# Performance work log

Measured on AMD Instinct MI355X. Metric: run time of the kernel, lower is better.

Reference implementation:

```python
import jax, jax.numpy as jnp
import numpy as np

EMBED_DIM = 768
NUM_HEADS = 12
HEAD_DIM = EMBED_DIM // NUM_HEADS  # 64
SEGMENT_LENGTHS = (2048, 4096, 8192)
DILATION_RATES = (1, 2, 4)
LN_EPS = 1e-5


def setup_inputs() -> dict:
    key = jax.random.key(0)
    ks = jax.random.split(key, 8)
    B, N, E = 2, 8192, EMBED_DIM
    std = 1.0 / np.sqrt(E)
    return {
        "query": jax.random.normal(ks[0], (B, N, E), jnp.float32),
        "key": jax.random.normal(ks[1], (B, N, E), jnp.float32),
        "value": jax.random.normal(ks[2], (B, N, E), jnp.float32),
        "Wqkv": jax.random.normal(ks[3], (3 * E, E), jnp.float32) * std,
        "bqkv": jnp.zeros((3 * E,), jnp.float32),
        "Wo": jax.random.normal(ks[4], (E, E), jnp.float32) * std,
        "bo": jnp.zeros((E,), jnp.float32),
        "ln_w": jnp.ones((E,), jnp.float32),
        "ln_b": jnp.zeros((E,), jnp.float32),
        "is_causal": 0,
    }


def _dilated_attention(q, k, v, is_causal):
    # q, k, v: (b, n, h, d). Heads are partitioned into len(SEGMENT_LENGTHS) groups.
    b, n, h, d = q.shape
    ng = len(SEGMENT_LENGTHS)
    g = h // ng  # heads per group
    scale = 1.0 / np.sqrt(d)
    outs = []
    for i, (s, r) in enumerate(zip(SEGMENT_LENGTHS, DILATION_RATES)):
        off = i % r
        hs = slice(i * g, (i + 1) * g)
        m = n // s          # number of segments
        t = (s - off + r - 1) // r  # dilated tokens per segment
        # (b, m, s, g, d) -> dilated subsample -> (b, m, t, g, d)
        qi = q[:, :, hs].reshape(b, m, s, g, d)[:, :, off::r] * scale
        ki = k[:, :, hs].reshape(b, m, s, g, d)[:, :, off::r]
        vi = v[:, :, hs].reshape(b, m, s, g, d)[:, :, off::r]
        # attention within each segment over the dilated tokens
        scores = jnp.einsum("bmqhd,bmkhd->bmhqk", qi, ki)  # (b,m,g,t,t)
        if is_causal:
            mask = jnp.tril(jnp.ones((t, t), bool))
            scores = jnp.where(mask, scores, jnp.finfo(scores.dtype).min)
        attn = jax.nn.softmax(scores, axis=-1)
        xi = jnp.einsum("bmhqk,bmkhd->bmqhd", attn, vi)  # (b,m,t,g,d)
        # scatter back into full segment positions (zeros elsewhere)
        full = jnp.zeros((b, m, s, g, d), xi.dtype).at[:, :, off::r].set(xi)
        outs.append(full.reshape(b, n, g, d))
    return jnp.concatenate(outs, axis=2)  # (b, n, h, d)


def reference(query, key, value, Wqkv, bqkv, Wo, bo, ln_w, ln_b, is_causal):
    b, n, e = query.shape
    h, d = NUM_HEADS, HEAD_DIM
    q = (query @ Wqkv[:e].T + bqkv[:e]).reshape(b, n, h, d)
    k = (key @ Wqkv[e:2 * e].T + bqkv[e:2 * e]).reshape(b, n, h, d)
    v = (value @ Wqkv[2 * e:].T + bqkv[2 * e:]).reshape(b, n, h, d)
    x = _dilated_attention(q, k, v, is_causal).reshape(b, n, e)
    # LayerNorm
    mu = jnp.mean(x, axis=-1, keepdims=True)
    var = jnp.mean(jnp.square(x - mu), axis=-1, keepdims=True)
    x = (x - mu) * jax.lax.rsqrt(var + LN_EPS) * ln_w + ln_b
    return x @ Wo.T + bo
```

## Files before the change

### kernel.cpp

```cpp
#include <hip/hip_runtime.h>
#include <stdint.h>
#include <stddef.h>

typedef __bf16 bf16;
typedef __attribute__((ext_vector_type(4))) float f32x4;
typedef __attribute__((ext_vector_type(16))) float f32x16;
typedef __attribute__((ext_vector_type(8))) bf16 bf16x8;
typedef __attribute__((ext_vector_type(4))) bf16 bf16x4;

#define INST_STRIDE (2048 * 64)

static __device__ __forceinline__ f32x4 mfma16(bf16x8 a, bf16x8 b, f32x4 c) {
  return __builtin_amdgcn_mfma_f32_16x16x32_bf16(a, b, c, 0, 0, 0);
}
static __device__ __forceinline__ f32x16 mfma32(bf16x8 a, bf16x8 b, f32x16 c) {
  return __builtin_amdgcn_mfma_f32_32x32x16_bf16(a, b, c, 0, 0, 0);
}
static __device__ __forceinline__ void gload16(const void* g, void* l) {
  __builtin_amdgcn_global_load_lds(
      (const __attribute__((address_space(1))) void*)g,
      (__attribute__((address_space(3))) void*)l, 16, 0, 0);
}

__global__ void convert_w(const float* __restrict__ Wqkv, const float* __restrict__ Wo,
                          bf16* __restrict__ wq, bf16* __restrict__ wo) {
  int idx = blockIdx.x * 256 + threadIdx.x;
  const int NQ = 3 * 768 * 768 / 4;
  const float4* src;
  bf16* dst;
  int i;
  if (idx < NQ) { src = (const float4*)Wqkv; dst = wq; i = idx; }
  else          { src = (const float4*)Wo;   dst = wo; i = idx - NQ; }
  float4 v = src[i];
  bf16x4 o = { (bf16)v.x, (bf16)v.y, (bf16)v.z, (bf16)v.w };
  *(bf16x4*)(dst + (size_t)i * 4) = o;
}

__launch_bounds__(512, 2)
__global__ void qkv_gemm(const float* __restrict__ Xq, const float* __restrict__ Xk,
                         const float* __restrict__ Xv, const bf16* __restrict__ Wb,
                         const float* __restrict__ bqkv, bf16* __restrict__ qg,
                         bf16* __restrict__ kg, bf16* __restrict__ vtg) {
  __shared__ __align__(16) bf16 lA[128 * 64];
  __shared__ __align__(16) bf16 lB[256 * 64];
  const int z = blockIdx.z;
  const float* __restrict__ X = (z == 0) ? Xq : ((z == 1) ? Xk : Xv);
  const int mt = blockIdx.x, nt = blockIdx.y;
  const int tid = threadIdx.x;
  const int lane = tid & 63, w = tid >> 6;
  const int wr = w >> 2, wc = w & 3;
  const int l15 = lane & 15, lg = lane >> 4;

  f32x4 acc[4][4];
#pragma unroll
  for (int i = 0; i < 4; ++i)
#pragma unroll
    for (int j = 0; j < 4; ++j) acc[i][j] = (f32x4){0.f, 0.f, 0.f, 0.f};

  for (int k0 = 0; k0 < 768; k0 += 64) {
#pragma unroll
    for (int j = 0; j < 4; ++j) {
      int region = w * 4 + j;
      int r = region * 8 + (lane >> 3);
      int c8 = lane & 7;
      const bf16* src = Wb + (size_t)(z * 768 + nt * 256 + r) * 768 + k0 + ((c8 ^ (r & 7)) << 3);
      gload16(src, (char*)lB + region * 1024);
    }
#pragma unroll
    for (int i = 0; i < 2; ++i) {
      int c = i * 512 + tid;
      int r = c >> 3, c8 = c & 7;
      const float* src = X + (size_t)(mt * 128 + r) * 768 + k0 + c8 * 8;
      float4 v0 = ((const float4*)src)[0];
      float4 v1 = ((const float4*)src)[1];
      bf16x8 o = { (bf16)v0.x, (bf16)v0.y, (bf16)v0.z, (bf16)v0.w,
                   (bf16)v1.x, (bf16)v1.y, (bf16)v1.z, (bf16)v1.w };
      *(bf16x8*)((char*)lA + r * 128 + ((c8 ^ (r & 7)) << 4)) = o;
    }
    __syncthreads();
#pragma unroll
    for (int ks = 0; ks < 2; ++ks) {
      bf16x8 af[4], bfr[4];
#pragma unroll
      for (int i = 0; i < 4; ++i) {
        int row = wr * 64 + i * 16 + l15;
        af[i] = *(const bf16x8*)((const char*)lA + row * 128 + (((ks * 4 + lg) ^ (row & 7)) << 4));
        int col = wc * 64 + i * 16 + l15;
        bfr[i] = *(const bf16x8*)((const char*)lB + col * 128 + (((ks * 4 + lg) ^ (col & 7)) << 4));
      }
      __builtin_amdgcn_s_setprio(1);
#pragma unroll
      for (int i = 0; i < 4; ++i)
#pragma unroll
        for (int j = 0; j < 4; ++j) acc[i][j] = mfma16(af[i], bfr[j], acc[i][j]);
      __builtin_amdgcn_s_setprio(0);
    }
    __syncthreads();
  }
#pragma unroll
  for (int j = 0; j < 4; ++j) {
    int col = nt * 256 + wc * 64 + j * 16 + l15;
    float bias = bqkv[z * 768 + col];
    int head = col >> 6, d = col & 63;
    int grp = head >> 2, hg = head & 3;
    int sl = 11 + grp;
    int rmask = (1 << grp) - 1;
    int base = (grp == 2) ? 24 : (grp << 4);
    int nseg = 4 >> grp;
#pragma unroll
    for (int i = 0; i < 4; ++i) {
      int row0 = mt * 128 + wr * 64 + i * 16 + (lg << 2);
#pragma unroll
      for (int reg = 0; reg < 4; ++reg) {
        int row = row0 + reg;
        float v = acc[i][j][reg] + bias;
        int bb = row >> 13, n = row & 8191;
        int pos = n & ((1 << sl) - 1), seg = n >> sl;
        int rel = pos - grp;
        if (rel >= 0 && (rel & rmask) == 0) {
          int tq = rel >> grp;
          size_t io = (size_t)(bb * 28 + base + hg * nseg + seg) * INST_STRIDE;
          if (z == 0) {
            qg[io + tq * 64 + d] = (bf16)(v * 0.125f);
          } else if (z == 1) {
            int dsw = (d & 7) | (((d >> 3) ^ (tq & 7)) << 3);
            kg[io + tq * 64 + dsw] = (bf16)v;
          } else {
            int tsw = (tq & ~63) | ((((tq >> 3) & 7) ^ (d & 7)) << 3) | (tq & 7);
            vtg[io + d * 2048 + tsw] = (bf16)v;
          }
        }
      }
    }
  }
}

#define CVTPK(lo_, hi_, out_) \
  asm("v_cvt_pk_bf16_f32 %0, %1, %2" : "=v"(out_) : "v"(lo_), "v"(hi_))

#define MAKE_PA(sv, kb2, dst)                                              \
  do {                                                                     \
    float p0 = __expf(sv[kb2 * 8 + 0] - m);                                \
    float p1 = __expf(sv[kb2 * 8 + 1] - m);                                \
    float p2 = __expf(sv[kb2 * 8 + 2] - m);                                \
    float p3 = __expf(sv[kb2 * 8 + 3] - m);                                \
    float p4 = __expf(sv[kb2 * 8 + 4] - m);                                \
    float p5 = __expf(sv[kb2 * 8 + 5] - m);                                \
    float p6 = __expf(sv[kb2 * 8 + 6] - m);                                \
    float p7 = __expf(sv[kb2 * 8 + 7] - m);                                \
    rs += (p0 + p1) + (p2 + p3) + ((p4 + p5) + (p6 + p7));                 \
    uint32_t a0, a1, a2, a3;                                               \
    CVTPK(p0, p1, a0); CVTPK(p2, p3, a1);                                  \
    CVTPK(p4, p5, a2); CVTPK(p6, p7, a3);                                  \
    asm("v_permlane32_swap_b32 %0, %1" : "+v"(a0), "+v"(a2));              \
    asm("v_permlane32_swap_b32 %0, %1" : "+v"(a1), "+v"(a3));              \
    union { uint32_t u[4]; bf16x8 v; } pk_;                                \
    pk_.u[0] = a0; pk_.u[1] = a1; pk_.u[2] = a2; pk_.u[3] = a3;            \
    dst = pk_.v;                                                           \
  } while (0)

__launch_bounds__(256, 2)
__global__ void attn(const bf16* __restrict__ qg, const bf16* __restrict__ kg,
                     const bf16* __restrict__ vtg, bf16* __restrict__ og,
                     const int* __restrict__ causal_p) {
  __shared__ __align__(16) bf16 lK[2][64 * 64];
  __shared__ __align__(16) bf16 lV[2][64 * 64];
  __shared__ float lSc[4][32];
  const int L = blockIdx.x + (blockIdx.y << 4);
  const int inst = (L & 7) * 7 + ((L >> 3) >> 4);
  const int qt = (L >> 3) & 15;
  const int tid = threadIdx.x, lane = tid & 63, w = tid >> 6;
  const int l31 = lane & 31, hi = lane >> 5;
  const int causal = causal_p[0];
  const size_t ib = (size_t)inst * INST_STRIDE;
  const int qbase = qt * 128 + w * 32;

  bf16x8 qf[4];
#pragma unroll
  for (int dt4 = 0; dt4 < 4; ++dt4)
    qf[dt4] = *(const bf16x8*)(qg + ib + (size_t)(qbase + l31) * 64 + dt4 * 16 + hi * 8);

  f32x16 oacc0 = {0}, oacc1 = {0};
  float m = -1e30f, l = 0.f;

#define STAGE(buf, kt_)                                                          \
  do {                                                                           \
    _Pragma("unroll") for (int j = 0; j < 2; ++j) {                              \
      int region = w * 2 + j;                                                    \
      int r = region * 8 + (lane >> 3);                                          \
      int c8 = lane & 7;                                                         \
      gload16(kg + ib + (size_t)((kt_) + r) * 64 + c8 * 8,                       \
              (char*)lK[buf] + region * 1024);                                   \
      gload16(vtg + ib + (size_t)r * 2048 + (kt_) + c8 * 8,                      \
              (char*)lV[buf] + region * 1024);                                   \
    }                                                                            \
  } while (0)

  STAGE(0, 0);
  __syncthreads();
  int cur = 0;
  for (int kt = 0; kt < 2048; kt += 64) {
    if (kt + 64 < 2048) STAGE(cur ^ 1, kt + 64);
    const bf16* K = lK[cur];
    const bf16* V = lV[cur];
    f32x16 st0 = {0}, st1 = {0};
    __builtin_amdgcn_s_setprio(1);
#pragma unroll
    for (int dt4 = 0; dt4 < 4; ++dt4) {
      int row0 = l31, row1 = 32 + l31;
      bf16x8 kf0 = *(const bf16x8*)((const char*)K + row0 * 128 + (((dt4 * 2 + hi) ^ (row0 & 7)) << 4));
      bf16x8 kf1 = *(const bf16x8*)((const char*)K + row1 * 128 + (((dt4 * 2 + hi) ^ (row1 & 7)) << 4));
      st0 = mfma32(kf0, qf[dt4], st0);
      st1 = mfma32(kf1, qf[dt4], st1);
    }
    __builtin_amdgcn_s_setprio(0);
    if (causal) {
      int q = qbase + l31;
#pragma unroll
      for (int r = 0; r < 16; ++r) {
        int kl = (r & 3) + 8 * (r >> 2) + 4 * hi;
        if (kt + kl > q) st0[r] = -1e30f;
        if (kt + 32 + kl > q) st1[r] = -1e30f;
      }
    }
    float pmax = st0[0];
#pragma unroll
    for (int r = 1; r < 16; ++r) pmax = fmaxf(pmax, st0[r]);
#pragma unroll
    for (int r = 0; r < 16; ++r) pmax = fmaxf(pmax, st1[r]);
    pmax = fmaxf(pmax, __shfl_xor(pmax, 32));
    if (!__all(pmax - m <= 8.f)) {
      float mnew = fmaxf(m, pmax);
      float scale = __expf(m - mnew);
      l *= scale;
      if (!hi) lSc[w][l31] = scale;
      asm volatile("s_waitcnt lgkmcnt(0)" ::: "memory");
      __builtin_amdgcn_sched_barrier(0);
#pragma unroll
      for (int r = 0; r < 16; ++r) {
        float sc = lSc[w][(r & 3) + 8 * (r >> 2) + 4 * hi];
        oacc0[r] *= sc;
        oacc1[r] *= sc;
      }
      m = mnew;
    }
    float rs = 0.f;
    bf16x8 pa0, pa1, pa2, pa3;
    MAKE_PA(st0, 0, pa0);
    MAKE_PA(st0, 1, pa1);
    MAKE_PA(st1, 0, pa2);
    MAKE_PA(st1, 1, pa3);
    rs += __shfl_xor(rs, 32);
    l += rs;
    __builtin_amdgcn_s_setprio(1);
#pragma unroll
    for (int kb = 0; kb < 4; ++kb) {
      bf16x8 pak = (kb == 0) ? pa0 : (kb == 1) ? pa1 : (kb == 2) ? pa2 : pa3;
      int r0 = l31, r1 = 32 + l31;
      bf16x8 vf0 = *(const bf16x8*)((const char*)V + r0 * 128 + (((kb * 2 + hi) ^ (r0 & 7)) << 4));
      bf16x8 vf1 = *(const bf16x8*)((const char*)V + r1 * 128 + (((kb * 2 + hi) ^ (r1 & 7)) << 4));
      oacc0 = mfma32(pak, vf0, oacc0);
      oacc1 = mfma32(pak, vf1, oacc1);
    }
    __builtin_amdgcn_s_setprio(0);
    __syncthreads();
    cur ^= 1;
  }
  if (!hi) lSc[w][l31] = 1.f / l;
  asm volatile("s_waitcnt lgkmcnt(0)" ::: "memory");
  __builtin_amdgcn_sched_barrier(0);
#pragma unroll
  for (int r = 0; r < 16; ++r) {
    int ql = (r & 3) + 8 * (r >> 2) + 4 * hi;
    float linv = lSc[w][ql];
    int q = qbase + ql;
    og[ib + (size_t)q * 64 + l31] = (bf16)(oacc0[r] * linv);
    og[ib + (size_t)q * 64 + 32 + l31] = (bf16)(oacc1[r] * linv);
  }
}

__global__ void ln_gather(const bf16* __restrict__ og, const float* __restrict__ lnw,
                          const float* __restrict__ lnb, bf16* __restrict__ xnorm) {
  const int tok = blockIdx.x * 4 + (threadIdx.x >> 6);
  const int lane = threadIdx.x & 63;
  const int bb = tok >> 13, n = tok & 8191;
  float vals[12];
#pragma unroll
  for (int h = 0; h < 12; ++h) {
    const int grp = h >> 2, hg = h & 3;
    const int sl = 11 + grp;
    int pos = n & ((1 << sl) - 1), seg = n >> sl;
    int rel = pos - grp;
    float v = 0.f;
    if (rel >= 0 && (rel & ((1 << grp) - 1)) == 0) {
      int tq = rel >> grp;
      int base = (grp == 2) ? 24 : (grp << 4);
      size_t inst = (size_t)(bb * 28 + base + hg * (4 >> grp) + seg);
      v = (float)og[inst * INST_STRIDE + (size_t)tq * 64 + lane];
    }
    vals[h] = v;
  }
  float sum = 0.f, sq = 0.f;
#pragma unroll
  for (int h = 0; h < 12; ++h) { sum += vals[h]; sq += vals[h] * vals[h]; }
#pragma unroll
  for (int mm = 32; mm; mm >>= 1) { sum += __shfl_xor(sum, mm); sq += __shfl_xor(sq, mm); }
  const float mu = sum * (1.f / 768.f);
  const float var = sq * (1.f / 768.f) - mu * mu;
  const float rstd = rsqrtf(var + 1e-5f);
  const int tok7 = tok & 7;
#pragma unroll
  for (int h = 0; h < 12; ++h) {
    int e = h * 64 + lane;
    float xn = (vals[h] - mu) * rstd * lnw[e] + lnb[e];
    int esw = h * 64 + ((((lane >> 3) ^ tok7) << 3) | (lane & 7));
    xnorm[(size_t)tok * 768 + esw] = (bf16)xn;
  }
}

__launch_bounds__(512, 2)
__global__ void out_gemm(const bf16* __restrict__ xn, const bf16* __restrict__ wo,
                         const float* __restrict__ bo, float* __restrict__ out) {
  __shared__ __align__(16) bf16 lA[128 * 64];
  __shared__ __align__(16) bf16 lB[256 * 64];
  const int mt = blockIdx.x, nt = blockIdx.y;
  const int tid = threadIdx.x, lane = tid & 63, w = tid >> 6;
  const int wr = w >> 2, wc = w & 3;
  const int l15 = lane & 15, lg = lane >> 4;
  f32x4 acc[4][4];
#pragma unroll
  for (int i = 0; i < 4; ++i)
#pragma unroll
    for (int j = 0; j < 4; ++j) acc[i][j] = (f32x4){0.f, 0.f, 0.f, 0.f};

  for (int k0 = 0; k0 < 768; k0 += 64) {
#pragma unroll
    for (int j = 0; j < 2; ++j) {
      int region = w * 2 + j;
      int r = region * 8 + (lane >> 3);
      int c8 = lane & 7;
      gload16(xn + (size_t)(mt * 128 + r) * 768 + k0 + c8 * 8, (char*)lA + region * 1024);
    }
#pragma unroll
    for (int j = 0; j < 4; ++j) {
      int region = w * 4 + j;
      int r = region * 8 + (lane >> 3);
      int c8 = lane & 7;
      gload16(wo + (size_t)(nt * 256 + r) * 768 + k0 + ((c8 ^ (r & 7)) << 3), (char*)lB + region * 1024);
    }
    __syncthreads();
#pragma unroll
    for (int ks = 0; ks < 2; ++ks) {
      bf16x8 af[4], bfr[4];
#pragma unroll
      for (int i = 0; i < 4; ++i) {
        int row = wr * 64 + i * 16 + l15;
        af[i] = *(const bf16x8*)((const char*)lA + row * 128 + (((ks * 4 + lg) ^ (row & 7)) << 4));
        int col = wc * 64 + i * 16 + l15;
        bfr[i] = *(const bf16x8*)((const char*)lB + col * 128 + (((ks * 4 + lg) ^ (col & 7)) << 4));
      }
      __builtin_amdgcn_s_setprio(1);
#pragma unroll
      for (int i = 0; i < 4; ++i)
#pragma unroll
        for (int j = 0; j < 4; ++j) acc[i][j] = mfma16(af[i], bfr[j], acc[i][j]);
      __builtin_amdgcn_s_setprio(0);
    }
    __syncthreads();
  }
#pragma unroll
  for (int j = 0; j < 4; ++j) {
    int col = nt * 256 + wc * 64 + j * 16 + l15;
    float bias = bo[col];
#pragma unroll
    for (int i = 0; i < 4; ++i) {
      int row0 = mt * 128 + wr * 64 + i * 16 + (lg << 2);
#pragma unroll
      for (int reg = 0; reg < 4; ++reg)
        out[(size_t)(row0 + reg) * 768 + col] = acc[i][j][reg] + bias;
    }
  }
}

extern "C" void kernel_launch(void* const* d_in, const int* in_sizes, int n_in,
                              void* d_out, int out_size, void* d_ws, size_t ws_size,
                              hipStream_t stream) {
  (void)in_sizes; (void)n_in; (void)out_size; (void)ws_size;
  const float* query = (const float*)d_in[0];
  const float* key_  = (const float*)d_in[1];
  const float* value = (const float*)d_in[2];
  const float* Wqkv  = (const float*)d_in[3];
  const float* bqkv  = (const float*)d_in[4];
  const float* Wo    = (const float*)d_in[5];
  const float* bo    = (const float*)d_in[6];
  const float* lnw   = (const float*)d_in[7];
  const float* lnb   = (const float*)d_in[8];
  const int* flag    = (const int*)d_in[9];
  float* out = (float*)d_out;

  char* ws = (char*)d_ws;
  size_t off = 0;
  auto alloc = [&](size_t bytes) -> char* {
    char* p = ws + off;
    off += (bytes + 255) & ~(size_t)255;
    return p;
  };
  bf16* wq_bf  = (bf16*)alloc((size_t)3 * 768 * 768 * 2);
  bf16* wo_bf  = (bf16*)alloc((size_t)768 * 768 * 2);
  bf16* qg     = (bf16*)alloc((size_t)56 * INST_STRIDE * 2);
  bf16* kg     = (bf16*)alloc((size_t)56 * INST_STRIDE * 2);
  bf16* vtg    = (bf16*)alloc((size_t)56 * INST_STRIDE * 2);
  bf16* og     = (bf16*)alloc((size_t)56 * INST_STRIDE * 2);
  bf16* xnorm  = (bf16*)alloc((size_t)16384 * 768 * 2);

  convert_w<<<dim3(2304), dim3(256), 0, stream>>>(Wqkv, Wo, wq_bf, wo_bf);
  qkv_gemm<<<dim3(128, 3, 3), dim3(512), 0, stream>>>(query, key_, value, wq_bf, bqkv, qg, kg, vtg);
  attn<<<dim3(16, 56), dim3(256), 0, stream>>>(qg, kg, vtg, og, flag);
  ln_gather<<<dim3(4096), dim3(256), 0, stream>>>(og, lnw, lnb, xnorm);
  out_gemm<<<dim3(128, 3), dim3(512), 0, stream>>>(xnorm, wo_bf, bo, out);
}
```

Before: 236.6 us.

## Double-buffer LDS in QKV and output GEMMs with 128x128 tiles

Both projection GEMMs now use ping-pong LDS buffers. The next K-tile's global loads are issued before computing on the current one, and the fp32 A-tile conversion for the next step is written to LDS after the current MFMAs. To fit the doubled buffers, the block tile shrinks from 128x256 with 512 threads to 128x128 with 256 threads, which doubles the grid. This is meant to hide global-load latency behind MFMA work, at the cost of more A-tile re-reads and extra registers holding prefetched float4 data.

```diff
diff --git a/kernel.cpp b/kernel.cpp
--- a/kernel.cpp
+++ b/kernel.cpp
@@ -36,19 +36,19 @@
   *(bf16x4*)(dst + (size_t)i * 4) = o;
 }
 
-__launch_bounds__(512, 2)
+__launch_bounds__(256, 2)
 __global__ void qkv_gemm(const float* __restrict__ Xq, const float* __restrict__ Xk,
                          const float* __restrict__ Xv, const bf16* __restrict__ Wb,
                          const float* __restrict__ bqkv, bf16* __restrict__ qg,
                          bf16* __restrict__ kg, bf16* __restrict__ vtg) {
-  __shared__ __align__(16) bf16 lA[128 * 64];
-  __shared__ __align__(16) bf16 lB[256 * 64];
+  __shared__ __align__(16) bf16 lA[2][128 * 64];
+  __shared__ __align__(16) bf16 lB[2][128 * 64];
   const int z = blockIdx.z;
   const float* __restrict__ X = (z == 0) ? Xq : ((z == 1) ? Xk : Xv);
   const int mt = blockIdx.x, nt = blockIdx.y;
   const int tid = threadIdx.x;
   const int lane = tid & 63, w = tid >> 6;
-  const int wr = w >> 2, wc = w & 3;
+  const int wr = w >> 1, wc = w & 1;
   const int l15 = lane & 15, lg = lane >> 4;
 
   f32x4 acc[4][4];
@@ -57,36 +57,55 @@
 #pragma unroll
     for (int j = 0; j < 4; ++j) acc[i][j] = (f32x4){0.f, 0.f, 0.f, 0.f};
 
-  for (int k0 = 0; k0 < 768; k0 += 64) {
+  float4 av[4][2];
+
+  auto ISSUE = [&](int t) {
+    int k0 = t * 64;
+#pragma unroll
+    for (int i = 0; i < 4; ++i) {
+      int c = i * 256 + tid;
+      int r = c >> 3, c8 = c & 7;
+      const float* src = X + (size_t)(mt * 128 + r) * 768 + k0 + c8 * 8;
+      av[i][0] = ((const float4*)src)[0];
+      av[i][1] = ((const float4*)src)[1];
+    }
 #pragma unroll
     for (int j = 0; j < 4; ++j) {
       int region = w * 4 + j;
       int r = region * 8 + (lane >> 3);
       int c8 = lane & 7;
-      const bf16* src = Wb + (size_t)(z * 768 + nt * 256 + r) * 768 + k0 + ((c8 ^ (r & 7)) << 3);
-      gload16(src, (char*)lB + region * 1024);
-    }
-#pragma unroll
-    for (int i = 0; i < 2; ++i) {
-      int c = i * 512 + tid;
+      const bf16* src = Wb + (size_t)(z * 768 + nt * 128 + r) * 768 + k0 + ((c8 ^ (r & 7)) << 3);
+      gload16(src, (char*)lB[t & 1] + region * 1024);
+    }
+  };
+  auto WRITE_A = [&](int t) {
+#pragma unroll
+    for (int i = 0; i < 4; ++i) {
+      int c = i * 256 + tid;
       int r = c >> 3, c8 = c & 7;
-      const float* src = X + (size_t)(mt * 128 + r) * 768 + k0 + c8 * 8;
-      float4 v0 = ((const float4*)src)[0];
-      float4 v1 = ((const float4*)src)[1];
+      float4 v0 = av[i][0], v1 = av[i][1];
       bf16x8 o = { (bf16)v0.x, (bf16)v0.y, (bf16)v0.z, (bf16)v0.w,
                    (bf16)v1.x, (bf16)v1.y, (bf16)v1.z, (bf16)v1.w };
-      *(bf16x8*)((char*)lA + r * 128 + ((c8 ^ (r & 7)) << 4)) = o;
-    }
-    __syncthreads();
+      *(bf16x8*)((char*)lA[t & 1] + r * 128 + ((c8 ^ (r & 7)) << 4)) = o;
+    }
+  };
+
+  ISSUE(0);
+  WRITE_A(0);
+  __syncthreads();
+  for (int t = 0; t < 12; ++t) {
+    if (t < 11) ISSUE(t + 1);
+    const char* pA = (const char*)lA[t & 1];
+    const char* pB = (const char*)lB[t & 1];
 #pragma unroll
     for (int ks = 0; ks < 2; ++ks) {
       bf16x8 af[4], bfr[4];
 #pragma unroll
       for (int i = 0; i < 4; ++i) {
         int row = wr * 64 + i * 16 + l15;
-        af[i] = *(const bf16x8*)((const char*)lA + row * 128 + (((ks * 4 + lg) ^ (row & 7)) << 4));
+        af[i] = *(const bf16x8*)(pA + row * 128 + (((ks * 4 + lg) ^ (row & 7)) << 4));
         int col = wc * 64 + i * 16 + l15;
-        bfr[i] = *(const bf16x8*)((const char*)lB + col * 128 + (((ks * 4 + lg) ^ (col & 7)) << 4));
+        bfr[i] = *(const bf16x8*)(pB + col * 128 + (((ks * 4 + lg) ^ (col & 7)) << 4));
       }
       __builtin_amdgcn_s_setprio(1);
 #pragma unroll
@@ -95,11 +114,12 @@
         for (int j = 0; j < 4; ++j) acc[i][j] = mfma16(af[i], bfr[j], acc[i][j]);
       __builtin_amdgcn_s_setprio(0);
     }
+    if (t < 11) WRITE_A(t + 1);
     __syncthreads();
   }
 #pragma unroll
   for (int j = 0; j < 4; ++j) {
-    int col = nt * 256 + wc * 64 + j * 16 + l15;
+    int col = nt * 128 + wc * 64 + j * 16 + l15;
     float bias = bqkv[z * 768 + col];
     int head = col >> 6, d = col & 63;
     int grp = head >> 2, hg = head & 3;
@@ -318,14 +338,14 @@
   }
 }
 
-__launch_bounds__(512, 2)
+__launch_bounds__(256, 2)
 __global__ void out_gemm(const bf16* __restrict__ xn, const bf16* __restrict__ wo,
                          const float* __restrict__ bo, float* __restrict__ out) {
-  __shared__ __align__(16) bf16 lA[128 * 64];
-  __shared__ __align__(16) bf16 lB[256 * 64];
+  __shared__ __align__(16) bf16 lA[2][128 * 64];
+  __shared__ __align__(16) bf16 lB[2][128 * 64];
   const int mt = blockIdx.x, nt = blockIdx.y;
   const int tid = threadIdx.x, lane = tid & 63, w = tid >> 6;
-  const int wr = w >> 2, wc = w & 3;
+  const int wr = w >> 1, wc = w & 1;
   const int l15 = lane & 15, lg = lane >> 4;
   f32x4 acc[4][4];
 #pragma unroll
@@ -333,31 +353,35 @@
 #pragma unroll
     for (int j = 0; j < 4; ++j) acc[i][j] = (f32x4){0.f, 0.f, 0.f, 0.f};
 
-  for (int k0 = 0; k0 < 768; k0 += 64) {
-#pragma unroll
-    for (int j = 0; j < 2; ++j) {
-      int region = w * 2 + j;
-      int r = region * 8 + (lane >> 3);
-      int c8 = lane & 7;
-      gload16(xn + (size_t)(mt * 128 + r) * 768 + k0 + c8 * 8, (char*)lA + region * 1024);
-    }
+  auto ISSUE = [&](int t) {
+    int k0 = t * 64;
 #pragma unroll
     for (int j = 0; j < 4; ++j) {
       int region = w * 4 + j;
       int r = region * 8 + (lane >> 3);
       int c8 = lane & 7;
-      gload16(wo + (size_t)(nt * 256 + r) * 768 + k0 + ((c8 ^ (r & 7)) << 3), (char*)lB + region * 1024);
-    }
-    __syncthreads();
+      gload16(xn + (size_t)(mt * 128 + r) * 768 + k0 + c8 * 8,
+              (char*)lA[t & 1] + region * 1024);
+      gload16(wo + (size_t)(nt * 128 + r) * 768 + k0 + ((c8 ^ (r & 7)) << 3),
+              (char*)lB[t & 1] + region * 1024);
+    }
+  };
+
+  ISSUE(0);
+  __syncthreads();
+  for (int t = 0; t < 12; ++t) {
+    if (t < 11) ISSUE(t + 1);
+    const char* pA = (const char*)lA[t & 1];
+    const char* pB = (const char*)lB[t & 1];
 #pragma unroll
     for (int ks = 0; ks < 2; ++ks) {
       bf16x8 af[4], bfr[4];
 #pragma unroll
       for (int i = 0; i < 4; ++i) {
         int row = wr * 64 + i * 16 + l15;
-        af[i] = *(const bf16x8*)((const char*)lA + row * 128 + (((ks * 4 + lg) ^ (row & 7)) << 4));
+        af[i] = *(const bf16x8*)(pA + row * 128 + (((ks * 4 + lg) ^ (row & 7)) << 4));
         int col = wc * 64 + i * 16 + l15;
-        bfr[i] = *(const bf16x8*)((const char*)lB + col * 128 + (((ks * 4 + lg) ^ (col & 7)) << 4));
+        bfr[i] = *(const bf16x8*)(pB + col * 128 + (((ks * 4 + lg) ^ (col & 7)) << 4));
       }
       __builtin_amdgcn_s_setprio(1);
 #pragma unroll
@@ -370,7 +394,7 @@
   }
 #pragma unroll
   for (int j = 0; j < 4; ++j) {
-    int col = nt * 256 + wc * 64 + j * 16 + l15;
+    int col = nt * 128 + wc * 64 + j * 16 + l15;
     float bias = bo[col];
 #pragma unroll
     for (int i = 0; i < 4; ++i) {
@@ -414,8 +438,8 @@
   bf16* xnorm  = (bf16*)alloc((size_t)16384 * 768 * 2);
 
   convert_w<<<dim3(2304), dim3(256), 0, stream>>>(Wqkv, Wo, wq_bf, wo_bf);
-  qkv_gemm<<<dim3(128, 3, 3), dim3(512), 0, stream>>>(query, key_, value, wq_bf, bqkv, qg, kg, vtg);
+  qkv_gemm<<<dim3(128, 6, 3), dim3(256), 0, stream>>>(query, key_, value, wq_bf, bqkv, qg, kg, vtg);
   attn<<<dim3(16, 56), dim3(256), 0, stream>>>(qg, kg, vtg, og, flag);
   ln_gather<<<dim3(4096), dim3(256), 0, stream>>>(og, lnw, lnb, xnorm);
-  out_gemm<<<dim3(128, 3), dim3(512), 0, stream>>>(xnorm, wo_bf, bo, out);
-}
+  out_gemm<<<dim3(128, 6), dim3(256), 0, stream>>>(xnorm, wo_bf, bo, out);
+}
```

Result: slower. 288.7 us (+22.0%).

## Double-buffer QKV and output GEMMs with async LDS loads and swizzled fp32 staging

Applied to the files above, without the earlier changes.

Both projection GEMMs now keep two LDS stages and prefetch tile t+2 while computing tile t, using explicit vmcnt waits and raw barriers in place of one synchronous load per iteration. The QKV GEMM loads fp32 activations straight into LDS through global_load_lds with an XOR swizzle and converts them to bf16 when building fragments, instead of converting in registers before the LDS write. LDS use grows to about 96KB per block for QKV, so the occupancy hint of 2 blocks is dropped. The xnorm swizzle moves out of the LayerNorm writer and into the out_gemm loader.

```diff
diff --git a/kernel.cpp b/kernel.cpp
--- a/kernel.cpp
+++ b/kernel.cpp
@@ -36,13 +36,13 @@
   *(bf16x4*)(dst + (size_t)i * 4) = o;
 }
 
-__launch_bounds__(512, 2)
+__launch_bounds__(512)
 __global__ void qkv_gemm(const float* __restrict__ Xq, const float* __restrict__ Xk,
                          const float* __restrict__ Xv, const bf16* __restrict__ Wb,
                          const float* __restrict__ bqkv, bf16* __restrict__ qg,
                          bf16* __restrict__ kg, bf16* __restrict__ vtg) {
-  __shared__ __align__(16) bf16 lA[128 * 64];
-  __shared__ __align__(16) bf16 lB[256 * 64];
+  __shared__ __align__(16) float lA[2][128 * 64];
+  __shared__ __align__(16) bf16  lB[2][256 * 64];
   const int z = blockIdx.z;
   const float* __restrict__ X = (z == 0) ? Xq : ((z == 1) ? Xk : Xv);
   const int mt = blockIdx.x, nt = blockIdx.y;
@@ -57,36 +57,48 @@
 #pragma unroll
     for (int j = 0; j < 4; ++j) acc[i][j] = (f32x4){0.f, 0.f, 0.f, 0.f};
 
-  for (int k0 = 0; k0 < 768; k0 += 64) {
-#pragma unroll
-    for (int j = 0; j < 4; ++j) {
-      int region = w * 4 + j;
-      int r = region * 8 + (lane >> 3);
+  auto STAGE = [&](int buf, int t) {
+#pragma unroll
+    for (int jj = 0; jj < 4; ++jj) {
+      int region = w * 4 + jj;
+      int row = region * 4 + (lane >> 4);
+      int g = lane & 15;
+      const float* src = X + (size_t)(mt * 128 + row) * 768 + t * 64 + ((g ^ (row & 15)) << 2);
+      gload16(src, (char*)lA[buf] + region * 1024);
+    }
+#pragma unroll
+    for (int jj = 0; jj < 4; ++jj) {
+      int region = w * 4 + jj;
+      int row = region * 8 + (lane >> 3);
       int c8 = lane & 7;
-      const bf16* src = Wb + (size_t)(z * 768 + nt * 256 + r) * 768 + k0 + ((c8 ^ (r & 7)) << 3);
-      gload16(src, (char*)lB + region * 1024);
-    }
-#pragma unroll
-    for (int i = 0; i < 2; ++i) {
-      int c = i * 512 + tid;
-      int r = c >> 3, c8 = c & 7;
-      const float* src = X + (size_t)(mt * 128 + r) * 768 + k0 + c8 * 8;
-      float4 v0 = ((const float4*)src)[0];
-      float4 v1 = ((const float4*)src)[1];
-      bf16x8 o = { (bf16)v0.x, (bf16)v0.y, (bf16)v0.z, (bf16)v0.w,
-                   (bf16)v1.x, (bf16)v1.y, (bf16)v1.z, (bf16)v1.w };
-      *(bf16x8*)((char*)lA + r * 128 + ((c8 ^ (r & 7)) << 4)) = o;
-    }
-    __syncthreads();
+      const bf16* src = Wb + (size_t)(z * 768 + nt * 256 + row) * 768 + t * 64 + ((c8 ^ (row & 7)) << 3);
+      gload16(src, (char*)lB[buf] + region * 1024);
+    }
+  };
+
+  STAGE(0, 0);
+  STAGE(1, 1);
+  for (int t = 0; t < 12; ++t) {
+    if (t < 11) asm volatile("s_waitcnt vmcnt(8)" ::: "memory");
+    else        asm volatile("s_waitcnt vmcnt(0)" ::: "memory");
+    __builtin_amdgcn_sched_barrier(0);
+    __builtin_amdgcn_s_barrier();
+    const float* pA = lA[t & 1];
+    const bf16*  pB = lB[t & 1];
 #pragma unroll
     for (int ks = 0; ks < 2; ++ks) {
       bf16x8 af[4], bfr[4];
 #pragma unroll
       for (int i = 0; i < 4; ++i) {
         int row = wr * 64 + i * 16 + l15;
-        af[i] = *(const bf16x8*)((const char*)lA + row * 128 + (((ks * 4 + lg) ^ (row & 7)) << 4));
+        int g0 = ks * 8 + lg * 2;
+        const char* base = (const char*)pA + row * 256;
+        f32x4 v0 = *(const f32x4*)(base + ((g0 ^ (row & 15)) << 4));
+        f32x4 v1 = *(const f32x4*)(base + (((g0 + 1) ^ (row & 15)) << 4));
+        af[i] = (bf16x8){ (bf16)v0[0], (bf16)v0[1], (bf16)v0[2], (bf16)v0[3],
+                          (bf16)v1[0], (bf16)v1[1], (bf16)v1[2], (bf16)v1[3] };
         int col = wc * 64 + i * 16 + l15;
-        bfr[i] = *(const bf16x8*)((const char*)lB + col * 128 + (((ks * 4 + lg) ^ (col & 7)) << 4));
+        bfr[i] = *(const bf16x8*)((const char*)pB + col * 128 + (((ks * 4 + lg) ^ (col & 7)) << 4));
       }
       __builtin_amdgcn_s_setprio(1);
 #pragma unroll
@@ -95,7 +107,9 @@
         for (int j = 0; j < 4; ++j) acc[i][j] = mfma16(af[i], bfr[j], acc[i][j]);
       __builtin_amdgcn_s_setprio(0);
     }
-    __syncthreads();
+    __builtin_amdgcn_sched_barrier(0);
+    __builtin_amdgcn_s_barrier();
+    if (t < 10) STAGE(t & 1, t + 2);
   }
 #pragma unroll
   for (int j = 0; j < 4; ++j) {
@@ -183,7 +197,7 @@
   f32x16 oacc0 = {0}, oacc1 = {0};
   float m = -1e30f, l = 0.f;
 
-#define STAGE(buf, kt_)                                                          \
+#define STAGE_AT(buf, kt_)                                                       \
   do {                                                                           \
     _Pragma("unroll") for (int j = 0; j < 2; ++j) {                              \
       int region = w * 2 + j;                                                    \
@@ -196,11 +210,11 @@
     }                                                                            \
   } while (0)
 
-  STAGE(0, 0);
+  STAGE_AT(0, 0);
   __syncthreads();
   int cur = 0;
   for (int kt = 0; kt < 2048; kt += 64) {
-    if (kt + 64 < 2048) STAGE(cur ^ 1, kt + 64);
+    if (kt + 64 < 2048) STAGE_AT(cur ^ 1, kt + 64);
     const bf16* K = lK[cur];
     const bf16* V = lV[cur];
     f32x16 st0 = {0}, st1 = {0};
@@ -308,21 +322,19 @@
   const float mu = sum * (1.f / 768.f);
   const float var = sq * (1.f / 768.f) - mu * mu;
   const float rstd = rsqrtf(var + 1e-5f);
-  const int tok7 = tok & 7;
 #pragma unroll
   for (int h = 0; h < 12; ++h) {
     int e = h * 64 + lane;
     float xn = (vals[h] - mu) * rstd * lnw[e] + lnb[e];
-    int esw = h * 64 + ((((lane >> 3) ^ tok7) << 3) | (lane & 7));
-    xnorm[(size_t)tok * 768 + esw] = (bf16)xn;
-  }
-}
-
-__launch_bounds__(512, 2)
+    xnorm[(size_t)tok * 768 + e] = (bf16)xn;
+  }
+}
+
+__launch_bounds__(512)
 __global__ void out_gemm(const bf16* __restrict__ xn, const bf16* __restrict__ wo,
                          const float* __restrict__ bo, float* __restrict__ out) {
-  __shared__ __align__(16) bf16 lA[128 * 64];
-  __shared__ __align__(16) bf16 lB[256 * 64];
+  __shared__ __align__(16) bf16 lA[2][128 * 64];
+  __shared__ __align__(16) bf16 lB[2][256 * 64];
   const int mt = blockIdx.x, nt = blockIdx.y;
   const int tid = threadIdx.x, lane = tid & 63, w = tid >> 6;
   const int wr = w >> 2, wc = w & 3;
@@ -333,31 +345,43 @@
 #pragma unroll
     for (int j = 0; j < 4; ++j) acc[i][j] = (f32x4){0.f, 0.f, 0.f, 0.f};
 
-  for (int k0 = 0; k0 < 768; k0 += 64) {
-#pragma unroll
-    for (int j = 0; j < 2; ++j) {
-      int region = w * 2 + j;
-      int r = region * 8 + (lane >> 3);
+  auto STAGE = [&](int buf, int t) {
+#pragma unroll
+    for (int jj = 0; jj < 2; ++jj) {
+      int region = w * 2 + jj;
+      int row = region * 8 + (lane >> 3);
       int c8 = lane & 7;
-      gload16(xn + (size_t)(mt * 128 + r) * 768 + k0 + c8 * 8, (char*)lA + region * 1024);
-    }
-#pragma unroll
-    for (int j = 0; j < 4; ++j) {
-      int region = w * 4 + j;
-      int r = region * 8 + (lane >> 3);
+      const bf16* src = xn + (size_t)(mt * 128 + row) * 768 + t * 64 + ((c8 ^ (row & 7)) << 3);
+      gload16(src, (char*)lA[buf] + region * 1024);
+    }
+#pragma unroll
+    for (int jj = 0; jj < 4; ++jj) {
+      int region = w * 4 + jj;
+      int row = region * 8 + (lane >> 3);
       int c8 = lane & 7;
-      gload16(wo + (size_t)(nt * 256 + r) * 768 + k0 + ((c8 ^ (r & 7)) << 3), (char*)lB + region * 1024);
-    }
-    __syncthreads();
+      const bf16* src = wo + (size_t)(nt * 256 + row) * 768 + t * 64 + ((c8 ^ (row & 7)) << 3);
+      gload16(src, (char*)lB[buf] + region * 1024);
+    }
+  };
+
+  STAGE(0, 0);
+  STAGE(1, 1);
+  for (int t = 0; t < 12; ++t) {
+    if (t < 11) asm volatile("s_waitcnt vmcnt(6)" ::: "memory");
+    else        asm volatile("s_waitcnt vmcnt(0)" ::: "memory");
+    __builtin_amdgcn_sched_barrier(0);
+    __builtin_amdgcn_s_barrier();
+    const bf16* pA = lA[t & 1];
+    const bf16* pB = lB[t & 1];
 #pragma unroll
     for (int ks = 0; ks < 2; ++ks) {
       bf16x8 af[4], bfr[4];
 #pragma unroll
       for (int i = 0; i < 4; ++i) {
         int row = wr * 64 + i * 16 + l15;
-        af[i] = *(const bf16x8*)((const char*)lA + row * 128 + (((ks * 4 + lg) ^ (row & 7)) << 4));
+        af[i] = *(const bf16x8*)((const char*)pA + row * 128 + (((ks * 4 + lg) ^ (row & 7)) << 4));
         int col = wc * 64 + i * 16 + l15;
-        bfr[i] = *(const bf16x8*)((const char*)lB + col * 128 + (((ks * 4 + lg) ^ (col & 7)) << 4));
+        bfr[i] = *(const bf16x8*)((const char*)pB + col * 128 + (((ks * 4 + lg) ^ (col & 7)) << 4));
       }
       __builtin_amdgcn_s_setprio(1);
 #pragma unroll
@@ -366,7 +390,9 @@
         for (int j = 0; j < 4; ++j) acc[i][j] = mfma16(af[i], bfr[j], acc[i][j]);
       __builtin_amdgcn_s_setprio(0);
     }
-    __syncthreads();
+    __builtin_amdgcn_sched_barrier(0);
+    __builtin_amdgcn_s_barrier();
+    if (t < 10) STAGE(t & 1, t + 2);
   }
 #pragma unroll
   for (int j = 0; j < 4; ++j) {
```

New measurement: 291.2 us. 23.1% more time.

## Project only dilated-sampled rows per head group in QKV GEMM

Applied to the files above, without the earlier changes.

The QKV projection previously computed all 16384 rows for every 256-column head group and then discarded rows not selected by the group's dilation. Each block now maps its tile to a head group and gathers only the input rows that group samples, so groups 1 and 2 compute a half and a quarter of the rows. The grid shrinks from 384 to 224 tiles per matrix, removing wasted MFMA work and wasted input loads. The cost is gathered, strided row reads of the fp32 input and some index arithmetic per row.

```diff
diff --git a/kernel.cpp b/kernel.cpp
--- a/kernel.cpp
+++ b/kernel.cpp
@@ -45,37 +45,62 @@
   __shared__ __align__(16) bf16 lB[256 * 64];
   const int z = blockIdx.z;
   const float* __restrict__ X = (z == 0) ? Xq : ((z == 1) ? Xk : Xv);
-  const int mt = blockIdx.x, nt = blockIdx.y;
+  const int bx = blockIdx.x;
+  int g, mt;
+  if (bx < 128)      { g = 0; mt = bx; }
+  else if (bx < 192) { g = 1; mt = bx - 128; }
+  else               { g = 2; mt = bx - 192; }
+  const int gshift = 13 - g;
+  const int gpbm = (8192 >> g) - 1;
+  const int ibase = (g == 2) ? 24 : (g << 4);
+  const int nseg = 4 >> g;
+
   const int tid = threadIdx.x;
   const int lane = tid & 63, w = tid >> 6;
   const int wr = w >> 2, wc = w & 3;
   const int l15 = lane & 15, lg = lane >> 4;
 
+  auto maprow = [&](int G) -> size_t {
+    int bb = G >> gshift;
+    int loc = G & gpbm;
+    int seg = loc >> 11, tq = loc & 2047;
+    int token = (seg << (11 + g)) + g + (tq << g);
+    return (size_t)(bb * 8192 + token);
+  };
+
+  const int c8 = tid & 7;
+  size_t arow[2];
+  int rr[2];
+#pragma unroll
+  for (int i = 0; i < 2; ++i) {
+    rr[i] = i * 64 + (tid >> 3);
+    arow[i] = maprow(mt * 128 + rr[i]);
+  }
+
   f32x4 acc[4][4];
 #pragma unroll
   for (int i = 0; i < 4; ++i)
 #pragma unroll
     for (int j = 0; j < 4; ++j) acc[i][j] = (f32x4){0.f, 0.f, 0.f, 0.f};
 
-  for (int k0 = 0; k0 < 768; k0 += 64) {
+  for (int t = 0; t < 12; ++t) {
+    const int k0 = t * 64;
 #pragma unroll
     for (int j = 0; j < 4; ++j) {
       int region = w * 4 + j;
-      int r = region * 8 + (lane >> 3);
-      int c8 = lane & 7;
-      const bf16* src = Wb + (size_t)(z * 768 + nt * 256 + r) * 768 + k0 + ((c8 ^ (r & 7)) << 3);
+      int row = region * 8 + (lane >> 3);
+      int cb = lane & 7;
+      const bf16* src = Wb + (size_t)(z * 768 + g * 256 + row) * 768 + k0 + ((cb ^ (row & 7)) << 3);
       gload16(src, (char*)lB + region * 1024);
     }
 #pragma unroll
     for (int i = 0; i < 2; ++i) {
-      int c = i * 512 + tid;
-      int r = c >> 3, c8 = c & 7;
-      const float* src = X + (size_t)(mt * 128 + r) * 768 + k0 + c8 * 8;
+      const float* src = X + arow[i] * 768 + k0 + c8 * 8;
       float4 v0 = ((const float4*)src)[0];
       float4 v1 = ((const float4*)src)[1];
       bf16x8 o = { (bf16)v0.x, (bf16)v0.y, (bf16)v0.z, (bf16)v0.w,
                    (bf16)v1.x, (bf16)v1.y, (bf16)v1.z, (bf16)v1.w };
-      *(bf16x8*)((char*)lA + r * 128 + ((c8 ^ (r & 7)) << 4)) = o;
+      *(bf16x8*)((char*)lA + rr[i] * 128 + ((c8 ^ (rr[i] & 7)) << 4)) = o;
     }
     __syncthreads();
 #pragma unroll
@@ -99,36 +124,29 @@
   }
 #pragma unroll
   for (int j = 0; j < 4; ++j) {
-    int col = nt * 256 + wc * 64 + j * 16 + l15;
-    float bias = bqkv[z * 768 + col];
-    int head = col >> 6, d = col & 63;
-    int grp = head >> 2, hg = head & 3;
-    int sl = 11 + grp;
-    int rmask = (1 << grp) - 1;
-    int base = (grp == 2) ? 24 : (grp << 4);
-    int nseg = 4 >> grp;
+    int col = wc * 64 + j * 16 + l15;
+    float bias = bqkv[z * 768 + g * 256 + col];
+    int hg = col >> 6, d = col & 63;
+    int ho = ibase + hg * nseg;
 #pragma unroll
     for (int i = 0; i < 4; ++i) {
-      int row0 = mt * 128 + wr * 64 + i * 16 + (lg << 2);
+      int G0 = mt * 128 + wr * 64 + i * 16 + (lg << 2);
 #pragma unroll
       for (int reg = 0; reg < 4; ++reg) {
-        int row = row0 + reg;
+        int G = G0 + reg;
+        int bb = G >> gshift;
+        int loc = G & gpbm;
+        int seg = loc >> 11, tq = loc & 2047;
+        size_t io = (size_t)(bb * 28 + ho + seg) * INST_STRIDE;
         float v = acc[i][j][reg] + bias;
-        int bb = row >> 13, n = row & 8191;
-        int pos = n & ((1 << sl) - 1), seg = n >> sl;
-        int rel = pos - grp;
-        if (rel >= 0 && (rel & rmask) == 0) {
-          int tq = rel >> grp;
-          size_t io = (size_t)(bb * 28 + base + hg * nseg + seg) * INST_STRIDE;
-          if (z == 0) {
-            qg[io + tq * 64 + d] = (bf16)(v * 0.125f);
-          } else if (z == 1) {
-            int dsw = (d & 7) | (((d >> 3) ^ (tq & 7)) << 3);
-            kg[io + tq * 64 + dsw] = (bf16)v;
-          } else {
-            int tsw = (tq & ~63) | ((((tq >> 3) & 7) ^ (d & 7)) << 3) | (tq & 7);
-            vtg[io + d * 2048 + tsw] = (bf16)v;
-          }
+        if (z == 0) {
+          qg[io + tq * 64 + d] = (bf16)(v * 0.125f);
+        } else if (z == 1) {
+          int dsw = (d & 7) | (((d >> 3) ^ (tq & 7)) << 3);
+          kg[io + tq * 64 + dsw] = (bf16)v;
+        } else {
+          int tsw = (tq & ~63) | ((((tq >> 3) & 7) ^ (d & 7)) << 3) | (tq & 7);
+          vtg[io + d * 2048 + tsw] = (bf16)v;
         }
       }
     }
@@ -183,24 +201,24 @@
   f32x16 oacc0 = {0}, oacc1 = {0};
   float m = -1e30f, l = 0.f;
 
-#define STAGE(buf, kt_)                                                          \
+#define STAGE_AT(buf, kt_)                                                       \
   do {                                                                           \
     _Pragma("unroll") for (int j = 0; j < 2; ++j) {                              \
       int region = w * 2 + j;                                                    \
       int r = region * 8 + (lane >> 3);                                          \
-      int c8 = lane & 7;                                                         \
-      gload16(kg + ib + (size_t)((kt_) + r) * 64 + c8 * 8,                       \
+      int cb = lane & 7;                                                         \
+      gload16(kg + ib + (size_t)((kt_) + r) * 64 + cb * 8,                       \
               (char*)lK[buf] + region * 1024);                                   \
-      gload16(vtg + ib + (size_t)r * 2048 + (kt_) + c8 * 8,                      \
+      gload16(vtg + ib + (size_t)r * 2048 + (kt_) + cb * 8,                      \
               (char*)lV[buf] + region * 1024);                                   \
     }                                                                            \
   } while (0)
 
-  STAGE(0, 0);
+  STAGE_AT(0, 0);
   __syncthreads();
   int cur = 0;
   for (int kt = 0; kt < 2048; kt += 64) {
-    if (kt + 64 < 2048) STAGE(cur ^ 1, kt + 64);
+    if (kt + 64 < 2048) STAGE_AT(cur ^ 1, kt + 64);
     const bf16* K = lK[cur];
     const bf16* V = lV[cur];
     f32x16 st0 = {0}, st1 = {0};
@@ -338,15 +356,15 @@
     for (int j = 0; j < 2; ++j) {
       int region = w * 2 + j;
       int r = region * 8 + (lane >> 3);
-      int c8 = lane & 7;
-      gload16(xn + (size_t)(mt * 128 + r) * 768 + k0 + c8 * 8, (char*)lA + region * 1024);
+      int cb = lane & 7;
+      gload16(xn + (size_t)(mt * 128 + r) * 768 + k0 + cb * 8, (char*)lA + region * 1024);
     }
 #pragma unroll
     for (int j = 0; j < 4; ++j) {
       int region = w * 4 + j;
       int r = region * 8 + (lane >> 3);
-      int c8 = lane & 7;
-      gload16(wo + (size_t)(nt * 256 + r) * 768 + k0 + ((c8 ^ (r & 7)) << 3), (char*)lB + region * 1024);
+      int cb = lane & 7;
+      gload16(wo + (size_t)(nt * 256 + r) * 768 + k0 + ((cb ^ (r & 7)) << 3), (char*)lB + region * 1024);
     }
     __syncthreads();
 #pragma unroll
@@ -414,7 +432,7 @@
   bf16* xnorm  = (bf16*)alloc((size_t)16384 * 768 * 2);
 
   convert_w<<<dim3(2304), dim3(256), 0, stream>>>(Wqkv, Wo, wq_bf, wo_bf);
-  qkv_gemm<<<dim3(128, 3, 3), dim3(512), 0, stream>>>(query, key_, value, wq_bf, bqkv, qg, kg, vtg);
+  qkv_gemm<<<dim3(224, 1, 3), dim3(512), 0, stream>>>(query, key_, value, wq_bf, bqkv, qg, kg, vtg);
   attn<<<dim3(16, 56), dim3(256), 0, stream>>>(qg, kg, vtg, og, flag);
   ln_gather<<<dim3(4096), dim3(256), 0, stream>>>(og, lnw, lnb, xnorm);
   out_gemm<<<dim3(128, 3), dim3(512), 0, stream>>>(xnorm, wo_bf, bo, out);
```

Result: no change. 233.4 us (-1.3%).
